# Optimization experiments

Hardware: AMD Instinct MI355X
Metric: run time of the kernel (lower is better)

## Reference

```python
import jax, jax.numpy as jnp
import numpy as np

NUM_NODES = 80000
V_GLOBALS = 50000
N = 32      # grapharea_size
D = 300     # feature dim
R = 4       # num relations
E = 64      # edges per timestep
B, T = 2, 64


def setup_inputs() -> dict:
    key = jax.random.key(0)
    ks = jax.random.split(key, 10)
    return {
        "x_indices": jax.random.randint(ks[0], (B, T, N), 0, NUM_NODES, dtype=jnp.int32),
        "edge_index": jax.random.randint(ks[1], (B, T, 2, E), 0, N, dtype=jnp.int32),
        "edge_type": jax.random.randint(ks[2], (B, T, E), 0, R, dtype=jnp.int32),
        "X": jax.random.normal(ks[3], (NUM_NODES, D), jnp.float32) * 0.1,
        "conv_W": jax.random.normal(ks[4], (R, D, D), jnp.float32) * (1.0 / np.sqrt(D)),
        "W_0": jax.random.normal(ks[5], (D, D), jnp.float32) * (1.0 / np.sqrt(D)),
        "update_gate_W": jax.random.normal(ks[6], (N * D, D), jnp.float32) * (1.0 / np.sqrt(N * D)),
        "update_gate_U": jax.random.normal(ks[7], (D, D), jnp.float32) * (1.0 / np.sqrt(D)),
        "lin_w": jax.random.normal(ks[8], (V_GLOBALS, D), jnp.float32) * (1.0 / np.sqrt(D)),
        "lin_b": jax.random.normal(ks[9], (V_GLOBALS,), jnp.float32) * 0.01,
    }


def _rgcn_step(X, conv_W, W_0, Wg, Ug, lin_w, lin_b, mem, idx, ei, et):
    # gather grapharea features: [N, D]
    gx = X[idx]
    src, dst = ei[0], ei[1]
    n = gx.shape[0]
    r = conv_W.shape[0]
    # per-relation linear transform: [R, N, D]
    xw = jnp.einsum('nd,rde->rne', gx, conv_W)
    # edge-type masks emulate split_edge_index: [R, E]
    mask = (et[None, :] == jnp.arange(r, dtype=et.dtype)[:, None]).astype(gx.dtype)
    # GCN symmetric normalization with self-loops (deg includes self-loop weight 1)
    deg = jax.vmap(lambda w: jax.ops.segment_sum(w, dst, num_segments=n))(mask) + 1.0  # [R, N]
    dis = jax.lax.rsqrt(deg)
    norm = dis[:, src] * dis[:, dst] * mask                      # [R, E]
    msgs = xw[:, src, :] * norm[..., None]                       # [R, E, D]
    agg = jax.vmap(lambda m: jax.ops.segment_sum(m, dst, num_segments=n))(msgs)
    agg = agg + xw * (dis ** 2)[..., None]                       # self-loop messages
    composite = agg.sum(0)                                       # sum over relations, [N, D]
    # eye(N) @ (gx @ W_0) == gx @ W_0
    proposed = composite + gx @ W_0
    # GRU-style update gate from flattened grapharea + previous memory's first node
    u = jax.nn.sigmoid(gx.reshape(-1) @ Wg + mem[0] @ Ug)        # [D]
    new = u[None, :] * proposed + (1.0 - u[None, :]) * mem       # [N, D]
    x1 = jax.nn.leaky_relu(new)[0]                               # current node, [D]
    logits = x1 @ lin_w.T + lin_b                                # [V]
    return new, jax.nn.log_softmax(logits)


def reference(x_indices, edge_index, edge_type, X, conv_W, W_0, update_gate_W, update_gate_U, lin_w, lin_b):
    b, t, n = x_indices.shape
    s = b * t
    idxs = x_indices.reshape(s, n)
    eis = edge_index.reshape(s, 2, -1)
    ets = edge_type.reshape(s, -1)

    def step(mem, inp):
        idx, ei, et = inp
        new, logp = _rgcn_step(X, conv_W, W_0, update_gate_W, update_gate_U,
                               lin_w, lin_b, mem, idx, ei, et)
        # memory carry is a non-grad buffer updated via .data.copy_ in torch
        return jax.lax.stop_gradient(new), logp

    mem0 = jnp.zeros((n, X.shape[1]), X.dtype)
    _, preds_globals = jax.lax.scan(step, mem0, (idxs, eis, ets))  # [S, V]
    preds_senses = jnp.zeros((s,), X.dtype)  # include_senses=False -> stacked zeros
    return preds_globals, preds_senses
```

## Files before the change

### kernel.cpp

```cpp
#include <hip/hip_runtime.h>

#define S 128
#define N 32
#define D 300
#define DP 320
#define E 64
#define R 4
#define V 50000
#define VP 50048
#define ND 9600
#define KY 1504
#define DPAD 304

typedef unsigned short ushortT;
typedef __attribute__((ext_vector_type(8))) short short8;
typedef __attribute__((ext_vector_type(4))) short short4v;
typedef __attribute__((ext_vector_type(4))) float floatx4;
typedef __attribute__((ext_vector_type(2))) _Float16 half2v;
typedef __attribute__((ext_vector_type(10))) unsigned int uintx10;

#if defined(__has_builtin)
#if __has_builtin(__builtin_amdgcn_fdot2)
#define HAVE_FDOT2 1
#endif
#endif

__device__ inline float bf2f(ushortT h) {
    unsigned u = ((unsigned)h) << 16;
    float f;
    __builtin_memcpy(&f, &u, 4);
    return f;
}

__device__ inline float bfbits_lo(unsigned u) {
    unsigned b = u << 16;
    float f;
    __builtin_memcpy(&f, &b, 4);
    return f;
}

__device__ inline float bfbits_hi(unsigned u) {
    unsigned b = u & 0xffff0000u;
    float f;
    __builtin_memcpy(&f, &b, 4);
    return f;
}

__device__ inline ushortT f2bf(float f) {
    unsigned u;
    __builtin_memcpy(&u, &f, 4);
    unsigned r = (u + 0x7fffu + ((u >> 16) & 1u)) >> 16;
    return (ushortT)r;
}

__device__ inline float ldf(const void* p, size_t i, int isb) {
    return isb ? bf2f(((const ushortT*)p)[i]) : ((const float*)p)[i];
}

__device__ inline float dot2f(unsigned a, unsigned b, float c) {
    half2v av, bv;
    __builtin_memcpy(&av, &a, 4);
    __builtin_memcpy(&bv, &b, 4);
#if defined(HAVE_FDOT2)
    return __builtin_amdgcn_fdot2(av, bv, c, false);
#else
    return fmaf((float)av[1], (float)bv[1], fmaf((float)av[0], (float)bv[0], c));
#endif
}

__device__ inline unsigned packh2(float lo, float hi) {
    half2v h;
    h[0] = (_Float16)lo;
    h[1] = (_Float16)hi;
    unsigned u;
    __builtin_memcpy(&u, &h, 4);
    return u;
}

__global__ void k_detect(const void* X, int* flag) {
    __shared__ int bad;
    if (threadIdx.x == 0) bad = 0;
    __syncthreads();
    const ushortT* p = (const ushortT*)X;
    int b = 0;
    for (int i = threadIdx.x; i < 4096; i += 256) {
        float v = bf2f(p[i]);
        if (!(v > -2.f && v < 2.f)) b = 1;
    }
    if (b) atomicOr(&bad, 1);
    __syncthreads();
    if (threadIdx.x == 0) flag[0] = bad ? 0 : 1;
}

__global__ void k_gatherb(const int* __restrict__ flag, const int* __restrict__ xi,
                          const void* __restrict__ X, ushortT* __restrict__ gxb) {
    int isb = flag[0];
    int sn = blockIdx.x;
    int d = threadIdx.x;
    if (d < D) {
        int node = xi[sn];
        ushortT v = isb ? ((const ushortT*)X)[(size_t)node * D + d]
                        : f2bf(((const float*)X)[(size_t)node * D + d]);
        gxb[(size_t)sn * D + d] = v;
    }
}

__global__ void k_twg(const int* __restrict__ flag, const void* __restrict__ Wg,
                      ushortT* __restrict__ wgt) {
    int isb = flag[0];
    __shared__ float tile[32][33];
    int k0 = blockIdx.x * 32, d0 = blockIdx.y * 32;
    int tx = threadIdx.x & 31, ty = threadIdx.x >> 5;
    for (int i = ty; i < 32; i += 8) {
        int d = d0 + tx;
        tile[i][tx] = (d < D) ? ldf(Wg, (size_t)(k0 + i) * D + d, isb) : 0.f;
    }
    __syncthreads();
    for (int i = ty; i < 32; i += 8) {
        int d = d0 + i;
        if (d < DPAD) wgt[(size_t)d * ND + k0 + tx] = f2bf(tile[tx][i]);
    }
}

__global__ void k_tws(const int* __restrict__ flag, const void* __restrict__ convW,
                      const void* __restrict__ W0, ushortT* __restrict__ wst) {
    int isb = flag[0];
    __shared__ float tile[32][33];
    int k0 = blockIdx.x * 32, d0 = blockIdx.y * 32;
    int tx = threadIdx.x & 31, ty = threadIdx.x >> 5;
    for (int i = ty; i < 32; i += 8) {
        int kp = k0 + i, d = d0 + tx;
        float v = 0.f;
        if (d < D && kp < 1500)
            v = (kp < 1200) ? ldf(convW, (size_t)kp * D + d, isb)
                            : ldf(W0, (size_t)(kp - 1200) * D + d, isb);
        tile[i][tx] = v;
    }
    __syncthreads();
    for (int i = ty; i < 32; i += 8) {
        int d = d0 + i;
        if (d < DPAD) wst[(size_t)d * KY + k0 + tx] = f2bf(tile[tx][i]);
    }
}

__global__ void k_yb(const ushortT* __restrict__ gxb, const int* __restrict__ ei,
                     const int* __restrict__ et, ushortT* __restrict__ yb) {
    int s = blockIdx.x;
    int t = threadIdx.x;
    __shared__ int se[E], de[E], te[E];
    __shared__ float disv[R][N];
    if (t < E) {
        se[t] = ei[(size_t)s * 2 * E + t];
        de[t] = ei[(size_t)s * 2 * E + E + t];
        te[t] = et[(size_t)s * E + t];
    }
    __syncthreads();
    if (t < R * N) {
        int r = t >> 5, n = t & 31;
        float c = 1.f;
        for (int e = 0; e < E; ++e) c += (te[e] == r && de[e] == n) ? 1.f : 0.f;
        disv[r][n] = rsqrtf(c);
    }
    __syncthreads();
    if (t < D) {
        const ushortT* g = gxb + (size_t)s * ND;
        float g0 = bf2f(g[t]);
        float yy[R];
#pragma unroll
        for (int r = 0; r < R; ++r) yy[r] = g0 * disv[r][0] * disv[r][0];
        for (int e = 0; e < E; ++e) {
            if (de[e] == 0) {
                int r = te[e];
                yy[r] += disv[r][se[e]] * disv[r][0] * bf2f(g[(size_t)se[e] * D + t]);
            }
        }
#pragma unroll
        for (int r = 0; r < R; ++r) yb[(size_t)s * KY + r * D + t] = f2bf(yy[r]);
        yb[(size_t)s * KY + 4 * D + t] = g[t];
    }
    if (t < 4) yb[(size_t)s * KY + 1500 + t] = 0;
}

__global__ __launch_bounds__(256) void k_gemm(const ushortT* __restrict__ A, int lda,
                                              const ushortT* __restrict__ Bt, int ldb,
                                              float* __restrict__ C, int ldc, int ncols,
                                              int kchunks, int per) {
    int wave = threadIdx.x >> 6, lane = threadIdx.x & 63;
    int col = lane & 15, quad = lane >> 4;
    int m0 = blockIdx.x * 16, n0 = blockIdx.y * 16;
    int z = blockIdx.z;
    int kbeg = z * per;
    int kend = kbeg + per;
    if (kend > kchunks) kend = kchunks;
    floatx4 acc = {0.f, 0.f, 0.f, 0.f};
    const ushortT* ap = A + (size_t)(m0 + col) * lda + quad * 8;
    const ushortT* bp = Bt + (size_t)(n0 + col) * ldb + quad * 8;
    for (int kc = kbeg + wave; kc < kend; kc += 4) {
        short8 a = *(const short8*)(ap + kc * 32);
        short8 b = *(const short8*)(bp + kc * 32);
        acc = __builtin_amdgcn_mfma_f32_16x16x32_bf16(a, b, acc, 0, 0, 0);
    }
    __shared__ float red[4][64][4];
#pragma unroll
    for (int i = 0; i < 4; ++i) red[wave][lane][i] = acc[i];
    __syncthreads();
    if (wave == 0) {
#pragma unroll
        for (int i = 0; i < 4; ++i) {
            float v = red[0][lane][i] + red[1][lane][i] + red[2][lane][i] + red[3][lane][i];
            int m = m0 + quad * 4 + i;
            int n = n0 + col;
            if (n < ncols) C[(size_t)z * S * ldc + (size_t)m * ldc + n] = v;
        }
    }
}

__global__ void k_red(const float* __restrict__ part, float* __restrict__ out, int n, int nz) {
    int i = blockIdx.x * 256 + threadIdx.x;
    if (i < n) {
        float v = 0.f;
        for (int z = 0; z < nz; ++z) v += part[(size_t)z * n + i];
        out[i] = v;
    }
}

__global__ __launch_bounds__(1024) void
k_scan(const int* __restrict__ flag, const float* __restrict__ a, const float* __restrict__ P0,
       const void* __restrict__ Ug, ushortT* __restrict__ x1p) {
    int isb = flag[0];
    int t = threadIdx.x;
    int w = t >> 6, lane = t & 63;
    int kbase = w * 20;
    int myk = kbase + lane;
    bool red_ok = (lane < 20) && (myk < D);
    int d4 = 256 + lane;
    bool d4ok = d4 < D;
    uintx10 UV0, UV1, UV2, UV3, UV4;
#pragma unroll
    for (int j = 0; j < 10; ++j) {
        int k1 = kbase + 2 * j, k2 = k1 + 1;
        bool k1ok = k1 < D, k2ok = k2 < D;
        UV0[j] = packh2(k1ok ? ldf(Ug, (size_t)k1 * D + lane, isb) : 0.f,
                        k2ok ? ldf(Ug, (size_t)k2 * D + lane, isb) : 0.f);
        UV1[j] = packh2(k1ok ? ldf(Ug, (size_t)k1 * D + 64 + lane, isb) : 0.f,
                        k2ok ? ldf(Ug, (size_t)k2 * D + 64 + lane, isb) : 0.f);
        UV2[j] = packh2(k1ok ? ldf(Ug, (size_t)k1 * D + 128 + lane, isb) : 0.f,
                        k2ok ? ldf(Ug, (size_t)k2 * D + 128 + lane, isb) : 0.f);
        UV3[j] = packh2(k1ok ? ldf(Ug, (size_t)k1 * D + 192 + lane, isb) : 0.f,
                        k2ok ? ldf(Ug, (size_t)k2 * D + 192 + lane, isb) : 0.f);
        UV4[j] = packh2((k1ok && d4ok) ? ldf(Ug, (size_t)k1 * D + d4, isb) : 0.f,
                        (k2ok && d4ok) ? ldf(Ug, (size_t)k2 * D + d4, isb) : 0.f);
    }
    for (int i = t; i < S * 20; i += 1024) {
        int s = i / 20, d = 300 + (i % 20);
        x1p[(size_t)s * DP + d] = 0;
    }
    __shared__ float part[2][16][320];
    __shared__ unsigned msh16[160];
    for (int i = t; i < 160; i += 1024) msh16[i] = 0;
    float mreg = 0.f;
    int buf = 0;
    __syncthreads();
    for (int s = 0; s < S; ++s) {
        float av = 0.f, pv = 0.f;
        if (red_ok) {
            av = a[s * D + myk];
            pv = P0[s * D + myk];
        }
        uintx10 MV;
#pragma unroll
        for (int j = 0; j < 10; ++j) MV[j] = msh16[w * 10 + j];
        float acc0 = 0.f, acc1 = 0.f, acc2 = 0.f, acc3 = 0.f, acc4 = 0.f;
#pragma unroll
        for (int j = 0; j < 10; ++j) {
            unsigned md = MV[j];
            acc0 = dot2f(UV0[j], md, acc0);
            acc1 = dot2f(UV1[j], md, acc1);
            acc2 = dot2f(UV2[j], md, acc2);
            acc3 = dot2f(UV3[j], md, acc3);
            acc4 = dot2f(UV4[j], md, acc4);
        }
        part[buf][w][lane] = acc0;
        part[buf][w][64 + lane] = acc1;
        part[buf][w][128 + lane] = acc2;
        part[buf][w][192 + lane] = acc3;
        part[buf][w][256 + lane] = acc4;
        __syncthreads();
        if (red_ok) {
            float q0 = part[buf][0][myk] + part[buf][1][myk];
            float q1 = part[buf][2][myk] + part[buf][3][myk];
            float q2 = part[buf][4][myk] + part[buf][5][myk];
            float q3 = part[buf][6][myk] + part[buf][7][myk];
            float q4 = part[buf][8][myk] + part[buf][9][myk];
            float q5 = part[buf][10][myk] + part[buf][11][myk];
            float q6 = part[buf][12][myk] + part[buf][13][myk];
            float q7 = part[buf][14][myk] + part[buf][15][myk];
            float r0 = q0 + q1, r1 = q2 + q3, r2 = q4 + q5, r3 = q6 + q7;
            float pr = av + ((r0 + r1) + (r2 + r3));
            float u = 1.f / (1.f + __expf(-pr));
            float nm = u * pv + (1.f - u) * mreg;
            mreg = nm;
            _Float16 mh = (_Float16)nm;
            ushortT mb;
            __builtin_memcpy(&mb, &mh, 2);
            ((ushortT*)msh16)[myk] = mb;
            float x = nm > 0.f ? nm : 0.01f * nm;
            x1p[(size_t)s * DP + myk] = f2bf(x);
        }
        buf ^= 1;
    }
}

__global__ __launch_bounds__(256) void k_logits(const int* __restrict__ flag,
                                                const ushortT* __restrict__ x1p,
                                                const void* __restrict__ lw,
                                                const void* __restrict__ lb,
                                                void* __restrict__ out) {
    int isb = flag[0];
    int wave = threadIdx.x >> 6, lane = threadIdx.x & 63;
    int col = lane & 15, quad = lane >> 4;
    int v = blockIdx.x * 64 + wave * 16 + col;
    int vv = v < V ? v : V - 1;
    floatx4 acc[8];
#pragma unroll
    for (int i = 0; i < 8; ++i) acc[i] = (floatx4){0.f, 0.f, 0.f, 0.f};
#pragma unroll
    for (int kc = 0; kc < 9; ++kc) {
        int k0 = kc * 32 + quad * 8;
        short8 b;
        if (isb) {
            const ushortT* bp = (const ushortT*)lw + (size_t)vv * D + k0;
            short4v lo = *(const short4v*)bp;
            short4v hi = *(const short4v*)(bp + 4);
            b = (short8){lo[0], lo[1], lo[2], lo[3], hi[0], hi[1], hi[2], hi[3]};
        } else {
            const float* bp = (const float*)lw + (size_t)vv * D + k0;
            floatx4 f0 = *(const floatx4*)bp;
            floatx4 f1 = *(const floatx4*)(bp + 4);
            b = (short8){(short)f2bf(f0[0]), (short)f2bf(f0[1]), (short)f2bf(f0[2]),
                         (short)f2bf(f0[3]), (short)f2bf(f1[0]), (short)f2bf(f1[1]),
                         (short)f2bf(f1[2]), (short)f2bf(f1[3])};
        }
#pragma unroll
        for (int st = 0; st < 8; ++st) {
            short8 aa = *(const short8*)(x1p + (size_t)(st * 16 + col) * DP + k0);
            acc[st] = __builtin_amdgcn_mfma_f32_16x16x32_bf16(aa, b, acc[st], 0, 0, 0);
        }
    }
    {
        int k0 = 288 + quad * 8;
        short8 b;
#pragma unroll
        for (int j = 0; j < 8; ++j) {
            int k = k0 + j;
            ushortT bv = 0;
            if (k < D)
                bv = isb ? ((const ushortT*)lw)[(size_t)vv * D + k]
                         : f2bf(((const float*)lw)[(size_t)vv * D + k]);
            b[j] = (short)bv;
        }
#pragma unroll
        for (int st = 0; st < 8; ++st) {
            short8 aa = *(const short8*)(x1p + (size_t)(st * 16 + col) * DP + k0);
            acc[st] = __builtin_amdgcn_mfma_f32_16x16x32_bf16(aa, b, acc[st], 0, 0, 0);
        }
    }
    if (v < V) {
        float bias = ldf(lb, v, isb);
#pragma unroll
        for (int st = 0; st < 8; ++st) {
#pragma unroll
            for (int i = 0; i < 4; ++i) {
                int s = st * 16 + quad * 4 + i;
                float val = acc[st][i] + bias;
                if (isb)
                    ((ushortT*)out)[(size_t)s * V + v] = f2bf(val);
                else
                    ((float*)out)[(size_t)s * V + v] = val;
            }
        }
    }
}

__global__ __launch_bounds__(512) void k_norm(const int* __restrict__ flag,
                                              void* __restrict__ out) {
    int isb = flag[0];
    int s = blockIdx.x;
    int t = threadIdx.x;
    __shared__ float red[512];
    if (s == 0 && t < S) {
        if (isb)
            ((ushortT*)out)[(size_t)S * V + t] = 0;
        else
            ((float*)out)[(size_t)S * V + t] = 0.f;
    }
    float mx = -1e30f;
    if (isb) {
        const uint4* row = (const uint4*)((const ushortT*)out + (size_t)s * V);
        for (int i = t; i < 6250; i += 512) {
            uint4 q = row[i];
            mx = fmaxf(mx, fmaxf(fmaxf(bfbits_lo(q.x), bfbits_hi(q.x)),
                                 fmaxf(bfbits_lo(q.y), bfbits_hi(q.y))));
            mx = fmaxf(mx, fmaxf(fmaxf(bfbits_lo(q.z), bfbits_hi(q.z)),
                                 fmaxf(bfbits_lo(q.w), bfbits_hi(q.w))));
        }
    } else {
        const floatx4* row = (const floatx4*)((const float*)out + (size_t)s * V);
        for (int i = t; i < 12500; i += 512) {
            floatx4 q = row[i];
            mx = fmaxf(mx, fmaxf(fmaxf(q[0], q[1]), fmaxf(q[2], q[3])));
        }
    }
    red[t] = mx;
    __syncthreads();
    for (int o = 256; o > 0; o >>= 1) {
        if (t < o) red[t] = fmaxf(red[t], red[t + o]);
        __syncthreads();
    }
    float M = red[0];
    __syncthreads();
    float sm = 0.f;
    if (isb) {
        const uint4* row = (const uint4*)((const ushortT*)out + (size_t)s * V);
        for (int i = t; i < 6250; i += 512) {
            uint4 q = row[i];
            sm += __expf(bfbits_lo(q.x) - M) + __expf(bfbits_hi(q.x) - M) +
                  __expf(bfbits_lo(q.y) - M) + __expf(bfbits_hi(q.y) - M) +
                  __expf(bfbits_lo(q.z) - M) + __expf(bfbits_hi(q.z) - M) +
                  __expf(bfbits_lo(q.w) - M) + __expf(bfbits_hi(q.w) - M);
        }
    } else {
        const floatx4* row = (const floatx4*)((const float*)out + (size_t)s * V);
        for (int i = t; i < 12500; i += 512) {
            floatx4 q = row[i];
            sm += __expf(q[0] - M) + __expf(q[1] - M) + __expf(q[2] - M) + __expf(q[3] - M);
        }
    }
    red[t] = sm;
    __syncthreads();
    for (int o = 256; o > 0; o >>= 1) {
        if (t < o) red[t] += red[t + o];
        __syncthreads();
    }
    float lse = M + __logf(red[0]);
    if (isb) {
        uint4* row = (uint4*)((ushortT*)out + (size_t)s * V);
        for (int i = t; i < 6250; i += 512) {
            uint4 q = row[i];
            uint4 o;
            o.x = (unsigned)f2bf(bfbits_lo(q.x) - lse) |
                  ((unsigned)f2bf(bfbits_hi(q.x) - lse) << 16);
            o.y = (unsigned)f2bf(bfbits_lo(q.y) - lse) |
                  ((unsigned)f2bf(bfbits_hi(q.y) - lse) << 16);
            o.z = (unsigned)f2bf(bfbits_lo(q.z) - lse) |
                  ((unsigned)f2bf(bfbits_hi(q.z) - lse) << 16);
            o.w = (unsigned)f2bf(bfbits_lo(q.w) - lse) |
                  ((unsigned)f2bf(bfbits_hi(q.w) - lse) << 16);
            row[i] = o;
        }
    } else {
        floatx4* row = (floatx4*)((float*)out + (size_t)s * V);
        for (int i = t; i < 12500; i += 512) {
            floatx4 q = row[i];
            q[0] -= lse;
            q[1] -= lse;
            q[2] -= lse;
            q[3] -= lse;
            row[i] = q;
        }
    }
}

#define OFF_FLAG 0
#define OFF_GXB 256
#define OFF_WGT 2457856
#define OFF_WST 8294656
#define OFF_YB 9209088
#define OFF_A 9594112
#define OFF_P0 9747712
#define OFF_X1P 9901312
#define OFF_STATS 9983232
#define OFF_PART 9983744
#define PART_A_BYTES (4 * S * D * 4)
#define PART_P_BYTES (2 * S * D * 4)

extern "C" void kernel_launch(void* const* d_in, const int* in_sizes, int n_in, void* d_out,
                              int out_size, void* d_ws, size_t ws_size, hipStream_t stream) {
    const int* xi = (const int*)d_in[0];
    const int* ei = (const int*)d_in[1];
    const int* et = (const int*)d_in[2];
    const void* X = d_in[3];
    const void* convW = d_in[4];
    const void* W0 = d_in[5];
    const void* Wg = d_in[6];
    const void* Ug = d_in[7];
    const void* lw = d_in[8];
    const void* lb = d_in[9];
    char* ws = (char*)d_ws;

    int* flag = (int*)(ws + OFF_FLAG);
    ushortT* gxb = (ushortT*)(ws + OFF_GXB);
    ushortT* wgt = (ushortT*)(ws + OFF_WGT);
    ushortT* wst = (ushortT*)(ws + OFF_WST);
    ushortT* yb = (ushortT*)(ws + OFF_YB);
    float* a = (float*)(ws + OFF_A);
    float* P0 = (float*)(ws + OFF_P0);
    ushortT* x1p = (ushortT*)(ws + OFF_X1P);

    bool split = ws_size >= (size_t)(OFF_PART + PART_A_BYTES + PART_P_BYTES);
    int nza = split ? 4 : 1;
    int nzp = split ? 2 : 1;
    float* apart = split ? (float*)(ws + OFF_PART) : a;
    float* ppart = split ? (float*)(ws + OFF_PART + PART_A_BYTES) : P0;
    int pera = (ND / 32 + nza - 1) / nza;
    int perp = (KY / 32 + nzp - 1) / nzp;

    hipLaunchKernelGGL(k_detect, dim3(1), dim3(256), 0, stream, X, flag);
    hipLaunchKernelGGL(k_gatherb, dim3(S * N), dim3(DP), 0, stream, flag, xi, X, gxb);
    hipLaunchKernelGGL(k_twg, dim3(ND / 32, 10), dim3(256), 0, stream, flag, Wg, wgt);
    hipLaunchKernelGGL(k_tws, dim3(KY / 32, 10), dim3(256), 0, stream, flag, convW, W0, wst);
    hipLaunchKernelGGL(k_yb, dim3(S), dim3(DP), 0, stream, gxb, ei, et, yb);
    hipLaunchKernelGGL(k_gemm, dim3(S / 16, 19, nza), dim3(256), 0, stream, gxb, ND, wgt, ND,
                       apart, D, D, ND / 32, pera);
    if (split)
        hipLaunchKernelGGL(k_red, dim3((S * D + 255) / 256), dim3(256), 0, stream, apart, a,
                           S * D, nza);
    hipLaunchKernelGGL(k_gemm, dim3(S / 16, 19, nzp), dim3(256), 0, stream, yb, KY, wst, KY,
                       ppart, D, D, KY / 32, perp);
    if (split)
        hipLaunchKernelGGL(k_red, dim3((S * D + 255) / 256), dim3(256), 0, stream, ppart, P0,
                           S * D, nzp);
    hipLaunchKernelGGL(k_scan, dim3(1), dim3(1024), 0, stream, flag, a, P0, Ug, x1p);
    hipLaunchKernelGGL(k_logits, dim3(VP / 64), dim3(256), 0, stream, flag, x1p, lw, lb, d_out);
    hipLaunchKernelGGL(k_norm, dim3(S), dim3(512), 0, stream, flag, d_out);
}
```

Measured before the change: 445.2 us.

## Repartition recurrent scan over 12 waves with prefetched gate inputs

The sequential GRU-gate scan kernel moves from 16 waves handling 20 k-rows each to 12 waves handling 25 rows each. This cuts the cross-wave reduction per timestep from 16 partial rows to 12 and drops boundary checks. The next step's a/P0 values are now loaded one iteration ahead to hide global-load latency on the serial critical path. The memory vector's layout in shared memory is remapped to the padded 26-entries-per-wave scheme, and each wave does more dot work and holds more registers per step.

```diff
diff --git a/kernel.cpp b/kernel.cpp
--- a/kernel.cpp
+++ b/kernel.cpp
@@ -17,7 +17,7 @@
 typedef __attribute__((ext_vector_type(4))) short short4v;
 typedef __attribute__((ext_vector_type(4))) float floatx4;
 typedef __attribute__((ext_vector_type(2))) _Float16 half2v;
-typedef __attribute__((ext_vector_type(10))) unsigned int uintx10;
+typedef __attribute__((ext_vector_type(13))) unsigned int uintx13;
 
 #if defined(__has_builtin)
 #if __has_builtin(__builtin_amdgcn_fdot2)
@@ -224,55 +224,60 @@
     }
 }
 
-__global__ __launch_bounds__(1024) void
+__global__ __attribute__((amdgpu_flat_work_group_size(768, 768), amdgpu_waves_per_eu(2, 2))) void
 k_scan(const int* __restrict__ flag, const float* __restrict__ a, const float* __restrict__ P0,
        const void* __restrict__ Ug, ushortT* __restrict__ x1p) {
     int isb = flag[0];
     int t = threadIdx.x;
     int w = t >> 6, lane = t & 63;
-    int kbase = w * 20;
+    int kbase = w * 25;
     int myk = kbase + lane;
-    bool red_ok = (lane < 20) && (myk < D);
+    bool red_ok = lane < 25;
     int d4 = 256 + lane;
     bool d4ok = d4 < D;
-    uintx10 UV0, UV1, UV2, UV3, UV4;
-#pragma unroll
-    for (int j = 0; j < 10; ++j) {
+    uintx13 UV0, UV1, UV2, UV3, UV4;
+#pragma unroll
+    for (int j = 0; j < 13; ++j) {
         int k1 = kbase + 2 * j, k2 = k1 + 1;
-        bool k1ok = k1 < D, k2ok = k2 < D;
-        UV0[j] = packh2(k1ok ? ldf(Ug, (size_t)k1 * D + lane, isb) : 0.f,
+        bool k2ok = (2 * j + 1) < 25;
+        UV0[j] = packh2(ldf(Ug, (size_t)k1 * D + lane, isb),
                         k2ok ? ldf(Ug, (size_t)k2 * D + lane, isb) : 0.f);
-        UV1[j] = packh2(k1ok ? ldf(Ug, (size_t)k1 * D + 64 + lane, isb) : 0.f,
+        UV1[j] = packh2(ldf(Ug, (size_t)k1 * D + 64 + lane, isb),
                         k2ok ? ldf(Ug, (size_t)k2 * D + 64 + lane, isb) : 0.f);
-        UV2[j] = packh2(k1ok ? ldf(Ug, (size_t)k1 * D + 128 + lane, isb) : 0.f,
+        UV2[j] = packh2(ldf(Ug, (size_t)k1 * D + 128 + lane, isb),
                         k2ok ? ldf(Ug, (size_t)k2 * D + 128 + lane, isb) : 0.f);
-        UV3[j] = packh2(k1ok ? ldf(Ug, (size_t)k1 * D + 192 + lane, isb) : 0.f,
+        UV3[j] = packh2(ldf(Ug, (size_t)k1 * D + 192 + lane, isb),
                         k2ok ? ldf(Ug, (size_t)k2 * D + 192 + lane, isb) : 0.f);
-        UV4[j] = packh2((k1ok && d4ok) ? ldf(Ug, (size_t)k1 * D + d4, isb) : 0.f,
+        UV4[j] = packh2(d4ok ? ldf(Ug, (size_t)k1 * D + d4, isb) : 0.f,
                         (k2ok && d4ok) ? ldf(Ug, (size_t)k2 * D + d4, isb) : 0.f);
     }
-    for (int i = t; i < S * 20; i += 1024) {
+    for (int i = t; i < S * 20; i += 768) {
         int s = i / 20, d = 300 + (i % 20);
         x1p[(size_t)s * DP + d] = 0;
     }
-    __shared__ float part[2][16][320];
-    __shared__ unsigned msh16[160];
-    for (int i = t; i < 160; i += 1024) msh16[i] = 0;
+    __shared__ float part[2][12][320];
+    __shared__ unsigned msh16[12 * 13];
+    for (int i = t; i < 12 * 13; i += 768) msh16[i] = 0;
     float mreg = 0.f;
     int buf = 0;
+    float av = 0.f, pv = 0.f;
+    if (red_ok) {
+        av = a[myk];
+        pv = P0[myk];
+    }
     __syncthreads();
     for (int s = 0; s < S; ++s) {
-        float av = 0.f, pv = 0.f;
-        if (red_ok) {
-            av = a[s * D + myk];
-            pv = P0[s * D + myk];
-        }
-        uintx10 MV;
-#pragma unroll
-        for (int j = 0; j < 10; ++j) MV[j] = msh16[w * 10 + j];
+        float avn = 0.f, pvn = 0.f;
+        if (red_ok && s + 1 < S) {
+            avn = a[(size_t)(s + 1) * D + myk];
+            pvn = P0[(size_t)(s + 1) * D + myk];
+        }
+        uintx13 MV;
+#pragma unroll
+        for (int j = 0; j < 13; ++j) MV[j] = msh16[13 * w + j];
         float acc0 = 0.f, acc1 = 0.f, acc2 = 0.f, acc3 = 0.f, acc4 = 0.f;
 #pragma unroll
-        for (int j = 0; j < 10; ++j) {
+        for (int j = 0; j < 13; ++j) {
             unsigned md = MV[j];
             acc0 = dot2f(UV0[j], md, acc0);
             acc1 = dot2f(UV1[j], md, acc1);
@@ -293,20 +298,19 @@
             float q3 = part[buf][6][myk] + part[buf][7][myk];
             float q4 = part[buf][8][myk] + part[buf][9][myk];
             float q5 = part[buf][10][myk] + part[buf][11][myk];
-            float q6 = part[buf][12][myk] + part[buf][13][myk];
-            float q7 = part[buf][14][myk] + part[buf][15][myk];
-            float r0 = q0 + q1, r1 = q2 + q3, r2 = q4 + q5, r3 = q6 + q7;
-            float pr = av + ((r0 + r1) + (r2 + r3));
+            float pr = av + (((q0 + q1) + (q2 + q3)) + (q4 + q5));
             float u = 1.f / (1.f + __expf(-pr));
             float nm = u * pv + (1.f - u) * mreg;
             mreg = nm;
             _Float16 mh = (_Float16)nm;
             ushortT mb;
             __builtin_memcpy(&mb, &mh, 2);
-            ((ushortT*)msh16)[myk] = mb;
+            ((ushortT*)msh16)[26 * w + lane] = mb;
             float x = nm > 0.f ? nm : 0.01f * nm;
             x1p[(size_t)s * DP + myk] = f2bf(x);
         }
+        av = avn;
+        pv = pvn;
         buf ^= 1;
     }
 }
@@ -530,7 +534,7 @@
     if (split)
         hipLaunchKernelGGL(k_red, dim3((S * D + 255) / 256), dim3(256), 0, stream, ppart, P0,
                            S * D, nzp);
-    hipLaunchKernelGGL(k_scan, dim3(1), dim3(1024), 0, stream, flag, a, P0, Ug, x1p);
+    hipLaunchKernelGGL(k_scan, dim3(1), dim3(768), 0, stream, flag, a, P0, Ug, x1p);
     hipLaunchKernelGGL(k_logits, dim3(VP / 64), dim3(256), 0, stream, flag, x1p, lw, lb, d_out);
     hipLaunchKernelGGL(k_norm, dim3(S), dim3(512), 0, stream, flag, d_out);
 }
```

New measurement: 426.3 us. 4.2% less time.
